# Kernel tuning notes

Hardware: AMD Instinct MI355X
Metric: run time of the kernel (lower is better)

## Reference

```python
import math
import jax, jax.numpy as jnp
import numpy as np

B, T, FDIM, ODIM = 16, 16, 64, 8
NQ, LAYERS, DEGREE = 10, 2, 3
NA = 4                      # ceil(log2(T))
TOT = NQ + NA               # 14 total wires
NROTS = 4 * NQ * LAYERS     # 80 params per timestep
QROTS = 4 * NQ              # 40 (qff circuit, 1 layer)
C64 = jnp.complex64


def ry_mat(t):
    c = jnp.cos(0.5 * t).astype(C64)
    s = jnp.sin(0.5 * t).astype(C64)
    return jnp.stack([jnp.stack([c, -s], -1), jnp.stack([s, c], -1)], -2)


def rz_mat(t):
    p = jnp.exp(-0.5j * t.astype(C64))
    q = jnp.exp(0.5j * t.astype(C64))
    z = jnp.zeros_like(p)
    return jnp.stack([jnp.stack([p, z], -1), jnp.stack([z, q], -1)], -2)


def crx_mat(t):
    c = jnp.cos(0.5 * t).astype(C64)
    s = (-1j) * jnp.sin(0.5 * t).astype(C64)
    z = jnp.zeros_like(c)
    o = jnp.ones_like(c)
    r0 = jnp.stack([o, z, z, z], -1)
    r1 = jnp.stack([z, o, z, z], -1)
    r2 = jnp.stack([z, z, c, s], -1)
    r3 = jnp.stack([z, z, s, c], -1)
    return jnp.stack([r0, r1, r2, r3], -2)


CNOT = jnp.array([[1, 0, 0, 0], [0, 1, 0, 0], [0, 0, 0, 1], [0, 0, 1, 0]], dtype=C64)


def apply_gate(state, U, wires):
    # state: (Be, 2,...,2) tensor; wire w lives on axis w+1. U: (2^k,2^k) or (Be,2^k,2^k)
    k = len(wires)
    axes = [w + 1 for w in wires]
    st = jnp.moveaxis(state, axes, list(range(1, k + 1)))
    shp = st.shape
    st = st.reshape(shp[0], 2 ** k, -1)
    eq = 'bij,bjr->bir' if U.ndim == 3 else 'ij,bjr->bir'
    st = jnp.einsum(eq, U, st).reshape(shp)
    return jnp.moveaxis(st, list(range(1, k + 1)), axes)


def sim14_seq(nq, layers):
    # gate sequence of Sim et al. circuit 14: RY ring, CRX ring, RY ring, CRX counter-ring
    seq, idx = [], 0
    for _ in range(layers):
        for i in range(nq):
            seq.append(('ry', (i,), idx)); idx += 1
        for i in range(nq - 1, -1, -1):
            seq.append(('crx', (i, (i + 1) % nq), idx)); idx += 1
        for i in range(nq):
            seq.append(('ry', (i,), idx)); idx += 1
        for i in [nq - 1] + list(range(nq - 1)):
            seq.append(('crx', (i, (i - 1) % nq), idx)); idx += 1
    return seq


def apply_sim14(state, params, layers, adjoint=False):
    seq = sim14_seq(NQ, layers)
    if adjoint:
        seq = seq[::-1]
    sign = -1.0 if adjoint else 1.0
    for kind, w, pidx in seq:
        th = sign * params[..., pidx]
        U = ry_mat(th) if kind == 'ry' else crx_mat(th)
        state = apply_gate(state, U, list(w))
    return state


def apply_prepare(state, prep_p, adjoint=False):
    # learnable PREPARE ansatz on ancilla wires NQ..NQ+NA-1 (n_prep_layers == NA)
    seq = []
    for ly in range(NA):
        for qi in range(NA):
            seq.append(('ry', NQ + qi, (ly, qi, 0)))
            seq.append(('rz', NQ + qi, (ly, qi, 1)))
        for i in range(NA - 1):
            seq.append(('cnot', (NQ + i, NQ + i + 1), None))
    if adjoint:
        seq = seq[::-1]
    sign = -1.0 if adjoint else 1.0
    for kind, w, pix in seq:
        if kind == 'cnot':
            state = apply_gate(state, CNOT, list(w))
        else:
            th = sign * prep_p[pix]
            U = ry_mat(th) if kind == 'ry' else rz_mat(th)
            state = apply_gate(state, U, [w])
    return state


def pcphase(state, phi):
    # PennyLane PCPhase(phi, dim=2^NQ, wires=anc+main): e^{+i phi} on ancilla==0 subspace, e^{-i phi} elsewhere
    st = state.reshape(B, 2 ** NQ, 2 ** NA)
    ph = jnp.exp(1j * phi.astype(C64))
    vec = jnp.where(jnp.arange(2 ** NA) == 0, ph, jnp.conj(ph))
    return (st * vec).reshape((B,) + (2,) * TOT)


def apply_select(state, ts_params, adjoint=False):
    # Select: apply sim14(ts_params[:, j]) on main wires when ancilla register == j
    # (T == 2^NA so there is no identity padding). Vectorized over batch x ancilla index.
    st = state.reshape(B, 2 ** NQ, 2 ** NA)
    st = jnp.moveaxis(st, 2, 1).reshape((B * T,) + (2,) * NQ)
    st = apply_sim14(st, ts_params.reshape(B * T, NROTS), LAYERS, adjoint)
    st = st.reshape(B, 2 ** NA, 2 ** NQ)
    return jnp.moveaxis(st, 1, 2).reshape((B,) + (2,) * TOT)


def expvals(state):
    # <X_i>, <Y_i>, <Z_i> on main wires, order X0..X9, Y0..Y9, Z0..Z9
    xs, ys, zs = [], [], []
    for i in range(NQ):
        s = jnp.moveaxis(state, i + 1, 1).reshape(B, 2, -1)
        s0, s1 = s[:, 0], s[:, 1]
        c = jnp.sum(jnp.conj(s0) * s1, axis=-1)
        xs.append(2.0 * jnp.real(c))
        ys.append(2.0 * jnp.imag(c))
        zs.append(jnp.sum(jnp.abs(s0) ** 2 - jnp.abs(s1) ** 2, axis=-1))
    return jnp.stack(xs + ys + zs, axis=1).astype(jnp.float32)  # (B, 3*NQ)


def make_pe():
    pos = np.arange(T, dtype=np.float32)[:, None]
    div = np.exp(np.arange(0, FDIM, 2, dtype=np.float32) * -(math.log(10000.0) / FDIM))
    pe = np.zeros((T, FDIM), np.float32)
    pe[:, 0::2] = np.sin(pos * div)
    pe[:, 1::2] = np.cos(pos * div[:FDIM // 2])
    return jnp.asarray(pe)


def setup_inputs():
    key = jax.random.key(0)
    ks = jax.random.split(key, 8)
    return {
        'x': jax.random.normal(ks[0], (B, FDIM, T), jnp.float32),
        'W_fp': jax.random.normal(ks[1], (NROTS, FDIM), jnp.float32) / math.sqrt(FDIM),
        'b_fp': jnp.zeros((NROTS,), jnp.float32),
        'prep_p': 0.1 * jax.random.normal(ks[2], (NA, NA, 2), jnp.float32),
        'sig_ang': 0.1 * jax.random.normal(ks[3], (DEGREE + 1,), jnp.float32),
        'qff_p': jax.random.uniform(ks[4], (QROTS,), jnp.float32),
        'W_out': jax.random.normal(ks[5], (ODIM, 3 * NQ), jnp.float32) / math.sqrt(3 * NQ),
        'b_out': jnp.zeros((ODIM,), jnp.float32),
    }


def reference(x, W_fp, b_fp, prep_p, sig_ang, qff_p, W_out, b_out):
    h = jnp.transpose(x, (0, 2, 1)) + make_pe()[None]          # (B, T, FDIM)
    ts = jax.nn.sigmoid(h @ W_fp.T + b_fp) * (2.0 * math.pi)    # (B, T, NROTS)
    # |0...0> on all 14 wires, batched
    psi = jnp.zeros((B, 2 ** TOT), C64).at[:, 0].set(1.0).reshape((B,) + (2,) * TOT)
    psi = pcphase(psi, sig_ang[0])
    for k in range(DEGREE):
        psi = apply_prepare(psi, prep_p, adjoint=False)
        psi = apply_select(psi, ts, adjoint=(k % 2 == 1))
        psi = apply_prepare(psi, prep_p, adjoint=True)
        psi = pcphase(psi, sig_ang[k + 1])
    psi = apply_sim14(psi, qff_p, layers=1, adjoint=False)      # QFF readout circuit
    exps = expvals(psi)                                         # (B, 30)
    return exps @ W_out.T + b_out                               # (B, ODIM)
```

## Files before the change

kernel.cpp:

```cpp
#include <hip/hip_runtime.h>
#include <math.h>
#include <utility>


typedef float v2f __attribute__((ext_vector_type(2)));

struct Gate { int ry; int tbit; int cbit; int pidx; };
struct GateTab { Gate g[40]; };

constexpr GateTab make_gates1() {
  GateTab tb{};
  int pos = 0, idx = 0;
  for (int i = 0; i < 10; ++i) { tb.g[pos] = Gate{1, 9 - i, -1, idx}; ++pos; ++idx; }
  for (int i = 9; i >= 0; --i) { tb.g[pos] = Gate{0, 9 - ((i + 1) % 10), 9 - i, idx}; ++pos; ++idx; }
  for (int i = 0; i < 10; ++i) { tb.g[pos] = Gate{1, 9 - i, -1, idx}; ++pos; ++idx; }
  for (int k = 0; k < 10; ++k) {
    int i = (k == 0) ? 9 : (k - 1);
    tb.g[pos] = Gate{0, 9 - ((i + 9) % 10), 9 - i, idx}; ++pos; ++idx;
  }
  return tb;
}
constexpr GateTab GTC = make_gates1();

__device__ __forceinline__ int insert_zero(int v, int p) {
  return ((v >> p) << (p + 1)) | (v & ((1 << p) - 1));
}
__device__ __forceinline__ float2 cmul(float2 A, float2 B) {
  return make_float2(A.x * B.x - A.y * B.y, A.x * B.y + A.y * B.x);
}
__device__ __forceinline__ float2 conj2(float2 A) { return make_float2(A.x, -A.y); }
__device__ __forceinline__ v2f vmk(float x, float y) { v2f r; r.x = x; r.y = y; return r; }

template<int XM>
__device__ __forceinline__ float lxor(float v) {
  if constexpr (XM == 1) {
    int r = __builtin_amdgcn_update_dpp(__float_as_int(v), __float_as_int(v),
                                        0xB1, 0xF, 0xF, true);
    return __int_as_float(r);
  } else if constexpr (XM == 2) {
    int r = __builtin_amdgcn_update_dpp(__float_as_int(v), __float_as_int(v),
                                        0x4E, 0xF, 0xF, true);
    return __int_as_float(r);
  } else if constexpr (XM == 8) {
    int r = __builtin_amdgcn_update_dpp(__float_as_int(v), __float_as_int(v),
                                        0x128, 0xF, 0xF, true);
    return __int_as_float(r);
  } else if constexpr (XM == 16) {
#if __has_builtin(__builtin_amdgcn_permlane16_swap)
    unsigned uv = __float_as_uint(v);
    auto r = __builtin_amdgcn_permlane16_swap(uv, uv, false, false);
    return __uint_as_float(r[0] ^ r[1] ^ uv);
#else
    return __shfl_xor(v, 16, 64);
#endif
  } else if constexpr (XM == 32) {
#if __has_builtin(__builtin_amdgcn_permlane32_swap)
    unsigned uv = __float_as_uint(v);
    auto r = __builtin_amdgcn_permlane32_swap(uv, uv, false, false);
    return __uint_as_float(r[0] ^ r[1] ^ uv);
#else
    return __shfl_xor(v, 32, 64);
#endif
  } else {
    return __shfl_xor(v, XM, 64);
  }
}
template<int XM>
__device__ __forceinline__ v2f lxor2(v2f v) {
  v2f r; r.x = lxor<XM>(v.x); r.y = lxor<XM>(v.y); return r;
}

__device__ __forceinline__ float wave_sum(float v) {
  v += lxor<1>(v);
  v += lxor<2>(v);
  v += lxor<4>(v);
  v += lxor<8>(v);
  v += lxor<16>(v);
  v += lxor<32>(v);
  return v;
}

struct alignas(128) GBar {
  unsigned cnt;
  unsigned gen;
  unsigned done;
  unsigned pad[29];
};
__device__ GBar g_gb[16];

__device__ __forceinline__ void group_barrier16(int b, int lane) {
  unsigned snap = __hip_atomic_load(&g_gb[b].gen, __ATOMIC_RELAXED, __HIP_MEMORY_SCOPE_AGENT);
  if (lane == 0) {
    unsigned old = __hip_atomic_fetch_add(&g_gb[b].cnt, 1u, __ATOMIC_ACQ_REL,
                                          __HIP_MEMORY_SCOPE_AGENT);
    if ((old & 15u) == 15u)
      __hip_atomic_store(&g_gb[b].gen, snap + 1u, __ATOMIC_RELEASE,
                         __HIP_MEMORY_SCOPE_AGENT);
  }
  while (__hip_atomic_load(&g_gb[b].gen, __ATOMIC_RELAXED, __HIP_MEMORY_SCOPE_AGENT) == snap)
    __builtin_amdgcn_s_sleep(1);
  (void)__hip_atomic_load(&g_gb[b].gen, __ATOMIC_ACQUIRE, __HIP_MEMORY_SCOPE_AGENT);
}

template<int P>
__device__ __forceinline__ void ry_gate(v2f (&a)[16], float c, float s, int lane) {
  if constexpr (P < 4) {
    constexpr int m = 1 << P;
#pragma unroll
    for (int r0 = 0; r0 < 16; ++r0) {
      if (!(r0 & m)) {
        int r1 = r0 | m;
        v2f a0 = a[r0], a1 = a[r1];
        a[r0] = c * a0 - s * a1;
        a[r1] = s * a0 + c * a1;
      }
    }
  } else {
    constexpr int xm = 1 << (P - 4);
    bool up = (lane >> (P - 4)) & 1;
    float sg = up ? s : -s;
#pragma unroll
    for (int r = 0; r < 16; ++r) {
      v2f wv = lxor2<xm>(a[r]);
      a[r] = c * a[r] + sg * wv;
    }
  }
}

template<int P, int Q>
__device__ __forceinline__ void crx_gate(v2f (&a)[16], float c, float s, int lane) {
  if constexpr (P < 4) {
    constexpr int m = 1 << P;
#pragma unroll
    for (int r0 = 0; r0 < 16; ++r0) {
      if (!(r0 & m)) {
        int r1 = r0 | m;
        bool act;
        if constexpr (Q < 4) act = (r0 >> Q) & 1;
        else act = (lane >> (Q - 4)) & 1;
        if (act) {
          v2f a0 = a[r0], a1 = a[r1];
          a[r0] = c * a0 + s * vmk(a1.y, -a1.x);
          a[r1] = c * a1 + s * vmk(a0.y, -a0.x);
        }
      }
    }
  } else {
    constexpr int xm = 1 << (P - 4);
#pragma unroll
    for (int r = 0; r < 16; ++r) {
      v2f wv = lxor2<xm>(a[r]);
      bool act;
      if constexpr (Q < 4) act = (r >> Q) & 1;
      else act = (lane >> (Q - 4)) & 1;
      if (act) a[r] = c * a[r] + s * vmk(wv.y, -wv.x);
    }
  }
}

template<bool ADJ, int G>
__device__ __forceinline__ void one_gate(v2f (&a)[16], const float2 (&sc)[40], int lane) {
  constexpr Gate g = GTC.g[ADJ ? (39 - G) : G];
  float2 scv = sc[g.pidx];
  float s = ADJ ? -scv.x : scv.x;
  float c = scv.y;
  if constexpr (g.ry != 0) ry_gate<g.tbit>(a, c, s, lane);
  else crx_gate<g.tbit, g.cbit>(a, c, s, lane);
}

template<bool ADJ, int... I>
__device__ __forceinline__ void run_layer_impl(v2f (&a)[16], const float2 (&sc)[40],
                                               int lane, std::integer_sequence<int, I...>) {
  (one_gate<ADJ, I>(a, sc, lane), ...);
}

template<bool ADJ>
__device__ __forceinline__ void run_layer(v2f (&a)[16], const float2* sc, int lane) {
  float2 rsc[40];
#pragma unroll
  for (int i = 0; i < 40; ++i) rsc[i] = sc[i];
  run_layer_impl<ADJ>(a, rsc, lane, std::make_integer_sequence<int, 40>{});
}

__global__ __launch_bounds__(256, 1) void k_fused(const float* __restrict__ x,
                                                  const float* __restrict__ W_fp,
                                                  const float* __restrict__ b_fp,
                                                  const float* __restrict__ prep,
                                                  const float* __restrict__ sig,
                                                  const float* __restrict__ qff,
                                                  const float* __restrict__ W_out,
                                                  const float* __restrict__ b_out,
                                                  float* __restrict__ out,
                                                  float4* __restrict__ part1,
                                                  float4* __restrict__ part2,
                                                  float* __restrict__ sv) {
  int blk = blockIdx.x;
  int b = blk >> 2, sub = blk & 3;
  int tid = threadIdx.x;
  int w = tid >> 6, lane = tid & 63;
  int aa = sub * 4 + w;

  __shared__ __align__(16) float h[4][64];
  __shared__ float2 scs[4][80];
  __shared__ float2 qscs[40];
  __shared__ float2 ps[32];
  __shared__ float2 es[4];
  __shared__ float2 u0s[16];
  __shared__ float4 R[2][512];

  if (sub == 0 && w == 0 && lane < 30) sv[b * 30 + lane] = 0.f;

  {
    int f = lane, k = f >> 1;
    float div = expf(-(float)(2 * k) * (logf(10000.f) / 64.f));
    float ang = (float)aa * div;
    float pe = (f & 1) ? cosf(ang) : sinf(ang);
    h[w][f] = x[(b * 64 + f) * 16 + aa] + pe;
  }
  if (w == 0) {
    if (lane < 32) {
      float s, c;
      sincosf(0.5f * prep[lane], &s, &c);
      ps[lane] = make_float2(s, c);
    } else if (lane < 36) {
      float s, c;
      sincosf(sig[lane - 32], &s, &c);
      es[lane - 32] = make_float2(c, s);
    }
  } else if (w == 1 && lane < 40) {
    float s, c;
    sincosf(0.5f * qff[lane], &s, &c);
    qscs[lane] = make_float2(s, c);
  }
  __syncthreads();

  if (w == 0) {
    float2 v[16];
#pragma unroll
    for (int i = 0; i < 16; ++i) v[i] = make_float2(i == 0 ? 1.f : 0.f, 0.f);
#pragma unroll 1
    for (int ly = 0; ly < 4; ++ly) {
#pragma unroll
      for (int qi = 0; qi < 4; ++qi) {
        int p = 3 - qi;
        float2 rc = ps[ly * 8 + qi * 2 + 0];
        {
          float s = rc.x, c = rc.y;
#pragma unroll
          for (int m = 0; m < 8; ++m) {
            int a0 = insert_zero(m, p), a1 = a0 | (1 << p);
            float2 t0 = v[a0], t1 = v[a1];
            v[a0] = make_float2(c * t0.x - s * t1.x, c * t0.y - s * t1.y);
            v[a1] = make_float2(s * t0.x + c * t1.x, s * t0.y + c * t1.y);
          }
        }
        rc = ps[ly * 8 + qi * 2 + 1];
        {
          float s = rc.x, c = rc.y;
#pragma unroll
          for (int m = 0; m < 8; ++m) {
            int a0 = insert_zero(m, p), a1 = a0 | (1 << p);
            float2 t0 = v[a0], t1 = v[a1];
            v[a0] = make_float2(c * t0.x + s * t0.y, c * t0.y - s * t0.x);
            v[a1] = make_float2(c * t1.x - s * t1.y, c * t1.y + s * t1.x);
          }
        }
      }
#pragma unroll
      for (int i = 0; i < 3; ++i) {
        int pc = 3 - i, pt = 2 - i;
#pragma unroll
        for (int m = 0; m < 4; ++m) {
          int mm = insert_zero(m, pt);
          mm = insert_zero(mm, pc);
          int a0 = mm | (1 << pc), a1 = a0 | (1 << pt);
          float2 t0 = v[a0], t1 = v[a1];
          v[a0] = t1; v[a1] = t0;
        }
      }
    }
    if (lane == 0) {
#pragma unroll
      for (int i = 0; i < 16; ++i) u0s[i] = v[i];
    }
  }

  {
    const float4* h4 = (const float4*)&h[w][0];
    for (int j = lane; j < 80; j += 64) {
      float acc = b_fp[j];
      const float4* w4 = (const float4*)(W_fp + j * 64);
#pragma unroll
      for (int k4 = 0; k4 < 16; ++k4) {
        float4 hh = h4[k4], ww = w4[k4];
        acc += hh.x * ww.x + hh.y * ww.y + hh.z * ww.z + hh.w * ww.w;
      }
      float sg = 1.f / (1.f + expf(-acc));
      float s, c;
      sincosf(sg * 3.14159265358979323846f, &s, &c);
      scs[w][j] = make_float2(s, c);
    }
  }
  __syncthreads();

  float2 u0aa = u0s[aa];
  float2 e0 = es[0], e1 = es[1], e2 = es[2];
  float2 m0  = cmul(u0aa, e0);
  float2 cu0 = conj2(u0aa);
  float2 ceA = conj2(e1);
  float2 wA  = make_float2(-2.f * e1.y * u0aa.y, 2.f * e1.y * u0aa.x);
  float2 ceB = conj2(e2);
  float2 wB  = make_float2(-2.f * e2.y * u0aa.y, 2.f * e2.y * u0aa.x);

  const float2* sc = &scs[w][0];
  v2f a[16];
#pragma unroll
  for (int r = 0; r < 16; ++r) a[r] = vmk(0.f, 0.f);
  if (lane == 0) a[0] = vmk(m0.x, m0.y);

#pragma unroll 1
  for (int ph = 0; ph < 7; ++ph) {
    if (ph == 2 || ph == 4) {
      float2 ce = (ph == 2) ? ceA : ceB;
      float2 wk = (ph == 2) ? wA : wB;
      float4* part = (ph == 2) ? part1 : part2;

      __syncthreads();
      if (w < 2) {
#pragma unroll
        for (int q = 0; q < 8; ++q) {
          float2 p0 = cmul(cu0, make_float2(a[2 * q].x, a[2 * q].y));
          float2 p1 = cmul(cu0, make_float2(a[2 * q + 1].x, a[2 * q + 1].y));
          R[w][q * 64 + lane] = make_float4(p0.x, p0.y, p1.x, p1.y);
        }
      }
      __syncthreads();
      if (w >= 2) {
#pragma unroll
        for (int q = 0; q < 8; ++q) {
          float4 v = R[w - 2][q * 64 + lane];
          float2 p0 = cmul(cu0, make_float2(a[2 * q].x, a[2 * q].y));
          float2 p1 = cmul(cu0, make_float2(a[2 * q + 1].x, a[2 * q + 1].y));
          R[w - 2][q * 64 + lane] =
              make_float4(v.x + p0.x, v.y + p0.y, v.z + p1.x, v.w + p1.y);
        }
      }
      __syncthreads();
#pragma unroll
      for (int qq = 0; qq < 2; ++qq) {
        int q = w * 2 + qq;
        float4 v0 = R[0][q * 64 + lane];
        float4 v1 = R[1][q * 64 + lane];
        part[(size_t)(b * 4 + sub) * 512 + q * 64 + lane] =
            make_float4(v0.x + v1.x, v0.y + v1.y, v0.z + v1.z, v0.w + v1.w);
      }
      group_barrier16(b, lane);

      float4 s4[8];
#pragma unroll
      for (int q = 0; q < 8; ++q) {
        float4 v0 = R[0][q * 64 + lane];
        float4 v1 = R[1][q * 64 + lane];
        s4[q] = make_float4(v0.x + v1.x, v0.y + v1.y, v0.z + v1.z, v0.w + v1.w);
      }
#pragma unroll 1
      for (int o = 1; o < 4; ++o) {
        int so = (sub + o) & 3;
        const float4* pp = part + (size_t)(b * 4 + so) * 512 + lane;
#pragma unroll
        for (int q = 0; q < 8; ++q) {
          float4 v = pp[q * 64];
          s4[q].x += v.x; s4[q].y += v.y; s4[q].z += v.z; s4[q].w += v.w;
        }
      }
#pragma unroll
      for (int q = 0; q < 8; ++q) {
        v2f a0 = a[2 * q], a1 = a[2 * q + 1];
        a[2 * q] = vmk(ce.x * a0.x - ce.y * a0.y + wk.x * s4[q].x - wk.y * s4[q].y,
                       ce.x * a0.y + ce.y * a0.x + wk.x * s4[q].y + wk.y * s4[q].x);
        a[2 * q + 1] = vmk(ce.x * a1.x - ce.y * a1.y + wk.x * s4[q].z - wk.y * s4[q].w,
                           ce.x * a1.y + ce.y * a1.x + wk.x * s4[q].w + wk.y * s4[q].z);
      }
    }
    const float2* scp;
    if (ph == 6) scp = &qscs[0];
    else scp = sc + ((ph == 1 || ph == 2 || ph == 5) ? 40 : 0);
    if (ph == 2 || ph == 3) run_layer<true>(a, scp, lane);
    else                    run_layer<false>(a, scp, lane);
  }

  {
    float obs[30];
#pragma unroll
    for (int p = 0; p <= 9; ++p) {
      int i = 9 - p;
      float cr = 0.f, ci = 0.f, zz = 0.f;
      if (p < 4) {
        int m = 1 << p;
#pragma unroll
        for (int r0 = 0; r0 < 16; ++r0) {
          if (!(r0 & m)) {
            v2f A0 = a[r0], A1 = a[r0 | m];
            cr += A0.x * A1.x + A0.y * A1.y;
            ci += A0.x * A1.y - A0.y * A1.x;
            zz += (A0.x * A0.x + A0.y * A0.y) - (A1.x * A1.x + A1.y * A1.y);
          }
        }
      } else {
        int xm = 1 << (p - 4);
        bool up = (lane >> (p - 4)) & 1;
#pragma unroll
        for (int r = 0; r < 16; ++r) {
          float wx = __shfl_xor(a[r].x, xm, 64);
          float wy = __shfl_xor(a[r].y, xm, 64);
          float n2 = a[r].x * a[r].x + a[r].y * a[r].y;
          if (!up) {
            cr += a[r].x * wx + a[r].y * wy;
            ci += a[r].x * wy - a[r].y * wx;
            zz += n2;
          } else {
            zz -= n2;
          }
        }
      }
      obs[i] = 2.f * cr;
      obs[10 + i] = 2.f * ci;
      obs[20 + i] = zz;
    }
#pragma unroll
    for (int j = 0; j < 30; ++j) obs[j] = wave_sum(obs[j]);

    float* Rf = (float*)R;
    __syncthreads();
    if (lane == 0) {
#pragma unroll
      for (int j = 0; j < 30; ++j) Rf[w * 30 + j] = obs[j];
    }
    __syncthreads();
    if (w == 0) {
      if (lane < 30) {
        float v = Rf[0 * 30 + lane] + Rf[1 * 30 + lane] +
                  Rf[2 * 30 + lane] + Rf[3 * 30 + lane];
        atomicAdd(&sv[b * 30 + lane], v);
      }
      int lastflag = 0;
      if (lane == 0) {
        unsigned old = __hip_atomic_fetch_add(&g_gb[b].done, 1u, __ATOMIC_ACQ_REL,
                                              __HIP_MEMORY_SCOPE_AGENT);
        lastflag = ((old & 3u) == 3u) ? 1 : 0;
      }
      lastflag = __shfl(lastflag, 0, 64);
      if (lastflag) {
        (void)__hip_atomic_load(&g_gb[b].done, __ATOMIC_ACQUIRE, __HIP_MEMORY_SCOPE_AGENT);
        if (lane < 8) {
          float acc = b_out[lane];
#pragma unroll
          for (int j = 0; j < 30; ++j) acc += W_out[lane * 30 + j] * sv[b * 30 + j];
          out[b * 8 + lane] = acc;
        }
      }
    }
  }
}

extern "C" void kernel_launch(void* const* d_in, const int* in_sizes, int n_in,
                              void* d_out, int out_size, void* d_ws, size_t ws_size,
                              hipStream_t stream) {
  const float* x     = (const float*)d_in[0];
  const float* W_fp  = (const float*)d_in[1];
  const float* b_fp  = (const float*)d_in[2];
  const float* prep  = (const float*)d_in[3];
  const float* sig   = (const float*)d_in[4];
  const float* qff   = (const float*)d_in[5];
  const float* W_out = (const float*)d_in[6];
  const float* b_out = (const float*)d_in[7];
  float* out = (float*)d_out;
  (void)in_sizes; (void)n_in; (void)out_size;

  char* ws = (char*)d_ws;
  const size_t SZ_PART = (size_t)64 * 512 * 16;
  float4* part1 = (float4*)ws;
  float4* part2 = (float4*)(ws + SZ_PART);
  float*  sv    = (float*)(ws + 2 * SZ_PART);
  (void)ws_size;

  k_fused<<<dim3(64), dim3(256), 0, stream>>>(x, W_fp, b_fp, prep, sig, qff,
                                              W_out, b_out, out, part1, part2, sv);
}
```

Baseline: 163.5 us.

## Split each 1024-amplitude state across two waves, doubling grid to 128 blocks

Each ancilla-branch state vector, previously held by one wave as 16 amplitudes per lane, is now split across a pair of waves with 8 amplitudes per lane. One qubit is mapped to the wave index, and gates on that qubit exchange amplitudes through double-buffered LDS with a block barrier. The grid doubles to 128 blocks, with a 32-way cross-block barrier per batch and 8-way partial-sum reduction. The per-wave compute and register pressure halve, at the cost of extra __syncthreads per wave-bit gate, a larger group barrier, and more global partial traffic. A ds_swizzle path is added for the xor-4 lane exchange.

```diff
diff --git a/kernel.cpp b/kernel.cpp
--- a/kernel.cpp
+++ b/kernel.cpp
@@ -22,6 +22,10 @@
 }
 constexpr GateTab GTC = make_gates1();
 
+constexpr int lanebit_of(int P) {
+  return P == 3 ? 0 : P == 4 ? 1 : P == 5 ? 2 : P == 7 ? 3 : P == 8 ? 4 : 5;
+}
+
 __device__ __forceinline__ int insert_zero(int v, int p) {
   return ((v >> p) << (p + 1)) | (v & ((1 << p) - 1));
 }
@@ -40,6 +44,9 @@
   } else if constexpr (XM == 2) {
     int r = __builtin_amdgcn_update_dpp(__float_as_int(v), __float_as_int(v),
                                         0x4E, 0xF, 0xF, true);
+    return __int_as_float(r);
+  } else if constexpr (XM == 4) {
+    int r = __builtin_amdgcn_ds_swizzle(__float_as_int(v), 0x101F);
     return __int_as_float(r);
   } else if constexpr (XM == 8) {
     int r = __builtin_amdgcn_update_dpp(__float_as_int(v), __float_as_int(v),
@@ -53,7 +60,7 @@
 #else
     return __shfl_xor(v, 16, 64);
 #endif
-  } else if constexpr (XM == 32) {
+  } else {
 #if __has_builtin(__builtin_amdgcn_permlane32_swap)
     unsigned uv = __float_as_uint(v);
     auto r = __builtin_amdgcn_permlane32_swap(uv, uv, false, false);
@@ -61,8 +68,6 @@
 #else
     return __shfl_xor(v, 32, 64);
 #endif
-  } else {
-    return __shfl_xor(v, XM, 64);
   }
 }
 template<int XM>
@@ -88,12 +93,12 @@
 };
 __device__ GBar g_gb[16];
 
-__device__ __forceinline__ void group_barrier16(int b, int lane) {
+__device__ __forceinline__ void group_barrier32(int b, int lane) {
   unsigned snap = __hip_atomic_load(&g_gb[b].gen, __ATOMIC_RELAXED, __HIP_MEMORY_SCOPE_AGENT);
   if (lane == 0) {
     unsigned old = __hip_atomic_fetch_add(&g_gb[b].cnt, 1u, __ATOMIC_ACQ_REL,
                                           __HIP_MEMORY_SCOPE_AGENT);
-    if ((old & 15u) == 15u)
+    if ((old & 31u) == 31u)
       __hip_atomic_store(&g_gb[b].gen, snap + 1u, __ATOMIC_RELEASE,
                          __HIP_MEMORY_SCOPE_AGENT);
   }
@@ -102,12 +107,35 @@
   (void)__hip_atomic_load(&g_gb[b].gen, __ATOMIC_ACQUIRE, __HIP_MEMORY_SCOPE_AGENT);
 }
 
+struct Ctx {
+  int lane, wbit;
+  int buf;
+  float2* xo0; float2* xo1;
+  const float2* xp0; const float2* xp1;
+};
+
+__device__ __forceinline__ const float2* xchg(v2f (&a)[8], Ctx& ctx) {
+  float2* wo = ctx.buf ? ctx.xo1 : ctx.xo0;
+#pragma unroll
+  for (int r = 0; r < 8; ++r) wo[r] = make_float2(a[r].x, a[r].y);
+  __syncthreads();
+  const float2* wp = ctx.buf ? ctx.xp1 : ctx.xp0;
+  ctx.buf ^= 1;
+  return wp;
+}
+
+template<int Q>
+__device__ __forceinline__ bool act_of(int r, int lane) {
+  if constexpr (Q < 3) return (r >> Q) & 1;
+  else { constexpr int lb = lanebit_of(Q); return (lane >> lb) & 1; }
+}
+
 template<int P>
-__device__ __forceinline__ void ry_gate(v2f (&a)[16], float c, float s, int lane) {
-  if constexpr (P < 4) {
+__device__ __forceinline__ void ry_gate(v2f (&a)[8], float c, float s, Ctx& ctx) {
+  if constexpr (P < 3) {
     constexpr int m = 1 << P;
 #pragma unroll
-    for (int r0 = 0; r0 < 16; ++r0) {
+    for (int r0 = 0; r0 < 8; ++r0) {
       if (!(r0 & m)) {
         int r1 = r0 | m;
         v2f a0 = a[r0], a1 = a[r1];
@@ -115,30 +143,69 @@
         a[r1] = s * a0 + c * a1;
       }
     }
+  } else if constexpr (P == 6) {
+    const float2* wp = xchg(a, ctx);
+    float sg = ctx.wbit ? s : -s;
+#pragma unroll
+    for (int r = 0; r < 8; ++r) {
+      float2 w = wp[r];
+      a[r] = c * a[r] + sg * vmk(w.x, w.y);
+    }
   } else {
-    constexpr int xm = 1 << (P - 4);
-    bool up = (lane >> (P - 4)) & 1;
+    constexpr int xm = 1 << lanebit_of(P);
+    bool up = (ctx.lane >> lanebit_of(P)) & 1;
     float sg = up ? s : -s;
 #pragma unroll
-    for (int r = 0; r < 16; ++r) {
+    for (int r = 0; r < 8; ++r) {
       v2f wv = lxor2<xm>(a[r]);
       a[r] = c * a[r] + sg * wv;
     }
   }
 }
 
-template<int P, int Q>
-__device__ __forceinline__ void crx_gate(v2f (&a)[16], float c, float s, int lane) {
-  if constexpr (P < 4) {
+template<int P>
+__device__ __forceinline__ void crx_all(v2f (&a)[8], float c, float s, Ctx& ctx) {
+  if constexpr (P < 3) {
     constexpr int m = 1 << P;
 #pragma unroll
-    for (int r0 = 0; r0 < 16; ++r0) {
+    for (int r0 = 0; r0 < 8; ++r0) {
       if (!(r0 & m)) {
         int r1 = r0 | m;
-        bool act;
-        if constexpr (Q < 4) act = (r0 >> Q) & 1;
-        else act = (lane >> (Q - 4)) & 1;
-        if (act) {
+        v2f a0 = a[r0], a1 = a[r1];
+        a[r0] = c * a0 + s * vmk(a1.y, -a1.x);
+        a[r1] = c * a1 + s * vmk(a0.y, -a0.x);
+      }
+    }
+  } else {
+    constexpr int xm = 1 << lanebit_of(P);
+#pragma unroll
+    for (int r = 0; r < 8; ++r) {
+      v2f wv = lxor2<xm>(a[r]);
+      a[r] = c * a[r] + s * vmk(wv.y, -wv.x);
+    }
+  }
+}
+
+template<int P, int Q>
+__device__ __forceinline__ void crx_gate(v2f (&a)[8], float c, float s, Ctx& ctx) {
+  if constexpr (Q == 6) {
+    if (ctx.wbit) crx_all<P>(a, c, s, ctx);
+  } else if constexpr (P == 6) {
+    const float2* wp = xchg(a, ctx);
+#pragma unroll
+    for (int r = 0; r < 8; ++r) {
+      if (act_of<Q>(r, ctx.lane)) {
+        float2 w = wp[r];
+        a[r] = c * a[r] + s * vmk(w.y, -w.x);
+      }
+    }
+  } else if constexpr (P < 3) {
+    constexpr int m = 1 << P;
+#pragma unroll
+    for (int r0 = 0; r0 < 8; ++r0) {
+      if (!(r0 & m)) {
+        int r1 = r0 | m;
+        if (act_of<Q>(r0, ctx.lane)) {
           v2f a0 = a[r0], a1 = a[r1];
           a[r0] = c * a0 + s * vmk(a1.y, -a1.x);
           a[r1] = c * a1 + s * vmk(a0.y, -a0.x);
@@ -146,40 +213,37 @@
       }
     }
   } else {
-    constexpr int xm = 1 << (P - 4);
-#pragma unroll
-    for (int r = 0; r < 16; ++r) {
+    constexpr int xm = 1 << lanebit_of(P);
+#pragma unroll
+    for (int r = 0; r < 8; ++r) {
       v2f wv = lxor2<xm>(a[r]);
-      bool act;
-      if constexpr (Q < 4) act = (r >> Q) & 1;
-      else act = (lane >> (Q - 4)) & 1;
-      if (act) a[r] = c * a[r] + s * vmk(wv.y, -wv.x);
+      if (act_of<Q>(r, ctx.lane)) a[r] = c * a[r] + s * vmk(wv.y, -wv.x);
     }
   }
 }
 
 template<bool ADJ, int G>
-__device__ __forceinline__ void one_gate(v2f (&a)[16], const float2 (&sc)[40], int lane) {
+__device__ __forceinline__ void one_gate(v2f (&a)[8], const float2 (&sc)[40], Ctx& ctx) {
   constexpr Gate g = GTC.g[ADJ ? (39 - G) : G];
   float2 scv = sc[g.pidx];
   float s = ADJ ? -scv.x : scv.x;
   float c = scv.y;
-  if constexpr (g.ry != 0) ry_gate<g.tbit>(a, c, s, lane);
-  else crx_gate<g.tbit, g.cbit>(a, c, s, lane);
+  if constexpr (g.ry != 0) ry_gate<g.tbit>(a, c, s, ctx);
+  else crx_gate<g.tbit, g.cbit>(a, c, s, ctx);
 }
 
 template<bool ADJ, int... I>
-__device__ __forceinline__ void run_layer_impl(v2f (&a)[16], const float2 (&sc)[40],
-                                               int lane, std::integer_sequence<int, I...>) {
-  (one_gate<ADJ, I>(a, sc, lane), ...);
+__device__ __forceinline__ void run_layer_impl(v2f (&a)[8], const float2 (&sc)[40],
+                                               Ctx& ctx, std::integer_sequence<int, I...>) {
+  (one_gate<ADJ, I>(a, sc, ctx), ...);
 }
 
 template<bool ADJ>
-__device__ __forceinline__ void run_layer(v2f (&a)[16], const float2* sc, int lane) {
+__device__ __forceinline__ void run_layer(v2f (&a)[8], const float2* sc, Ctx& ctx) {
   float2 rsc[40];
 #pragma unroll
   for (int i = 0; i < 40; ++i) rsc[i] = sc[i];
-  run_layer_impl<ADJ>(a, rsc, lane, std::make_integer_sequence<int, 40>{});
+  run_layer_impl<ADJ>(a, rsc, ctx, std::make_integer_sequence<int, 40>{});
 }
 
 __global__ __launch_bounds__(256, 1) void k_fused(const float* __restrict__ x,
@@ -195,42 +259,44 @@
                                                   float4* __restrict__ part2,
                                                   float* __restrict__ sv) {
   int blk = blockIdx.x;
-  int b = blk >> 2, sub = blk & 3;
+  int b = blk >> 3, sub = blk & 7;
   int tid = threadIdx.x;
   int w = tid >> 6, lane = tid & 63;
-  int aa = sub * 4 + w;
-
-  __shared__ __align__(16) float h[4][64];
-  __shared__ float2 scs[4][80];
+  int c = w >> 1, wbit = w & 1;
+  int aa = sub * 2 + c;
+
+  __shared__ float2 X[2][2][2][64][8];
+  __shared__ float2 R[1024];
+  __shared__ __align__(16) float h[2][64];
+  __shared__ float2 scs[2][80];
   __shared__ float2 qscs[40];
   __shared__ float2 ps[32];
   __shared__ float2 es[4];
   __shared__ float2 u0s[16];
-  __shared__ float4 R[2][512];
 
   if (sub == 0 && w == 0 && lane < 30) sv[b * 30 + lane] = 0.f;
 
-  {
+  if (wbit == 0) {
     int f = lane, k = f >> 1;
     float div = expf(-(float)(2 * k) * (logf(10000.f) / 64.f));
     float ang = (float)aa * div;
     float pe = (f & 1) ? cosf(ang) : sinf(ang);
-    h[w][f] = x[(b * 64 + f) * 16 + aa] + pe;
-  }
-  if (w == 0) {
+    h[c][f] = x[(b * 64 + f) * 16 + aa] + pe;
+  }
+  if (w == 1) {
     if (lane < 32) {
-      float s, c;
-      sincosf(0.5f * prep[lane], &s, &c);
-      ps[lane] = make_float2(s, c);
+      float s, cc;
+      sincosf(0.5f * prep[lane], &s, &cc);
+      ps[lane] = make_float2(s, cc);
     } else if (lane < 36) {
-      float s, c;
-      sincosf(sig[lane - 32], &s, &c);
-      es[lane - 32] = make_float2(c, s);
-    }
-  } else if (w == 1 && lane < 40) {
-    float s, c;
-    sincosf(0.5f * qff[lane], &s, &c);
-    qscs[lane] = make_float2(s, c);
+      float s, cc;
+      sincosf(sig[lane - 32], &s, &cc);
+      es[lane - 32] = make_float2(cc, s);
+    }
+  } else if (w == 3 && lane < 40) {
+    float s, cc;
+    sincosf(0.5f * qff[lane], &s, &cc);
+    qscs[lane] = make_float2(s, cc);
   }
   __syncthreads();
 
@@ -245,24 +311,24 @@
         int p = 3 - qi;
         float2 rc = ps[ly * 8 + qi * 2 + 0];
         {
-          float s = rc.x, c = rc.y;
+          float s = rc.x, cc = rc.y;
 #pragma unroll
           for (int m = 0; m < 8; ++m) {
             int a0 = insert_zero(m, p), a1 = a0 | (1 << p);
             float2 t0 = v[a0], t1 = v[a1];
-            v[a0] = make_float2(c * t0.x - s * t1.x, c * t0.y - s * t1.y);
-            v[a1] = make_float2(s * t0.x + c * t1.x, s * t0.y + c * t1.y);
+            v[a0] = make_float2(cc * t0.x - s * t1.x, cc * t0.y - s * t1.y);
+            v[a1] = make_float2(s * t0.x + cc * t1.x, s * t0.y + cc * t1.y);
           }
         }
         rc = ps[ly * 8 + qi * 2 + 1];
         {
-          float s = rc.x, c = rc.y;
+          float s = rc.x, cc = rc.y;
 #pragma unroll
           for (int m = 0; m < 8; ++m) {
             int a0 = insert_zero(m, p), a1 = a0 | (1 << p);
             float2 t0 = v[a0], t1 = v[a1];
-            v[a0] = make_float2(c * t0.x + s * t0.y, c * t0.y - s * t0.x);
-            v[a1] = make_float2(c * t1.x - s * t1.y, c * t1.y + s * t1.x);
+            v[a0] = make_float2(cc * t0.x + s * t0.y, cc * t0.y - s * t0.x);
+            v[a1] = make_float2(cc * t1.x - s * t1.y, cc * t1.y + s * t1.x);
           }
         }
       }
@@ -285,21 +351,20 @@
     }
   }
 
-  {
-    const float4* h4 = (const float4*)&h[w][0];
-    for (int j = lane; j < 80; j += 64) {
-      float acc = b_fp[j];
-      const float4* w4 = (const float4*)(W_fp + j * 64);
-#pragma unroll
-      for (int k4 = 0; k4 < 16; ++k4) {
-        float4 hh = h4[k4], ww = w4[k4];
-        acc += hh.x * ww.x + hh.y * ww.y + hh.z * ww.z + hh.w * ww.w;
-      }
-      float sg = 1.f / (1.f + expf(-acc));
-      float s, c;
-      sincosf(sg * 3.14159265358979323846f, &s, &c);
-      scs[w][j] = make_float2(s, c);
-    }
+  if (lane < 40) {
+    int j = wbit * 40 + lane;
+    const float4* h4 = (const float4*)&h[c][0];
+    float acc = b_fp[j];
+    const float4* w4 = (const float4*)(W_fp + j * 64);
+#pragma unroll
+    for (int k4 = 0; k4 < 16; ++k4) {
+      float4 hh = h4[k4], ww = w4[k4];
+      acc += hh.x * ww.x + hh.y * ww.y + hh.z * ww.z + hh.w * ww.w;
+    }
+    float sg = 1.f / (1.f + expf(-acc));
+    float s, cc;
+    sincosf(sg * 3.14159265358979323846f, &s, &cc);
+    scs[c][j] = make_float2(s, cc);
   }
   __syncthreads();
 
@@ -312,11 +377,18 @@
   float2 ceB = conj2(e2);
   float2 wB  = make_float2(-2.f * e2.y * u0aa.y, 2.f * e2.y * u0aa.x);
 
-  const float2* sc = &scs[w][0];
-  v2f a[16];
-#pragma unroll
-  for (int r = 0; r < 16; ++r) a[r] = vmk(0.f, 0.f);
-  if (lane == 0) a[0] = vmk(m0.x, m0.y);
+  Ctx ctx;
+  ctx.lane = lane; ctx.wbit = wbit; ctx.buf = 0;
+  ctx.xo0 = &X[c][0][wbit][lane][0];
+  ctx.xo1 = &X[c][1][wbit][lane][0];
+  ctx.xp0 = &X[c][0][wbit ^ 1][lane][0];
+  ctx.xp1 = &X[c][1][wbit ^ 1][lane][0];
+
+  const float2* sc = &scs[c][0];
+  v2f a[8];
+#pragma unroll
+  for (int r = 0; r < 8; ++r) a[r] = vmk(0.f, 0.f);
+  if (wbit == 0 && lane == 0) a[0] = vmk(m0.x, m0.y);
 
 #pragma unroll 1
   for (int ph = 0; ph < 7; ++ph) {
@@ -324,69 +396,62 @@
       float2 ce = (ph == 2) ? ceA : ceB;
       float2 wk = (ph == 2) ? wA : wB;
       float4* part = (ph == 2) ? part1 : part2;
+      int base = wbit * 512 + lane * 8;
 
       __syncthreads();
-      if (w < 2) {
-#pragma unroll
-        for (int q = 0; q < 8; ++q) {
-          float2 p0 = cmul(cu0, make_float2(a[2 * q].x, a[2 * q].y));
-          float2 p1 = cmul(cu0, make_float2(a[2 * q + 1].x, a[2 * q + 1].y));
-          R[w][q * 64 + lane] = make_float4(p0.x, p0.y, p1.x, p1.y);
-        }
+      if (c == 0) {
+#pragma unroll
+        for (int r = 0; r < 8; ++r)
+          R[base + r] = cmul(cu0, make_float2(a[r].x, a[r].y));
       }
       __syncthreads();
-      if (w >= 2) {
-#pragma unroll
-        for (int q = 0; q < 8; ++q) {
-          float4 v = R[w - 2][q * 64 + lane];
-          float2 p0 = cmul(cu0, make_float2(a[2 * q].x, a[2 * q].y));
-          float2 p1 = cmul(cu0, make_float2(a[2 * q + 1].x, a[2 * q + 1].y));
-          R[w - 2][q * 64 + lane] =
-              make_float4(v.x + p0.x, v.y + p0.y, v.z + p1.x, v.w + p1.y);
+      if (c == 1) {
+#pragma unroll
+        for (int r = 0; r < 8; ++r) {
+          float2 v = R[base + r];
+          float2 p = cmul(cu0, make_float2(a[r].x, a[r].y));
+          R[base + r] = make_float2(v.x + p.x, v.y + p.y);
         }
       }
       __syncthreads();
-#pragma unroll
-      for (int qq = 0; qq < 2; ++qq) {
-        int q = w * 2 + qq;
-        float4 v0 = R[0][q * 64 + lane];
-        float4 v1 = R[1][q * 64 + lane];
-        part[(size_t)(b * 4 + sub) * 512 + q * 64 + lane] =
-            make_float4(v0.x + v1.x, v0.y + v1.y, v0.z + v1.z, v0.w + v1.w);
-      }
-      group_barrier16(b, lane);
-
-      float4 s4[8];
-#pragma unroll
-      for (int q = 0; q < 8; ++q) {
-        float4 v0 = R[0][q * 64 + lane];
-        float4 v1 = R[1][q * 64 + lane];
-        s4[q] = make_float4(v0.x + v1.x, v0.y + v1.y, v0.z + v1.z, v0.w + v1.w);
+      {
+        float4* dst = part + (size_t)(b * 8 + sub) * 512;
+        const float4* src = (const float4*)R;
+        dst[tid] = src[tid];
+        dst[tid + 256] = src[tid + 256];
+      }
+      group_barrier32(b, lane);
+
+      float4 sA[4];
+#pragma unroll
+      for (int q = 0; q < 4; ++q) {
+        float2 lo = R[base + 2 * q], hi = R[base + 2 * q + 1];
+        sA[q] = make_float4(lo.x, lo.y, hi.x, hi.y);
       }
 #pragma unroll 1
-      for (int o = 1; o < 4; ++o) {
-        int so = (sub + o) & 3;
-        const float4* pp = part + (size_t)(b * 4 + so) * 512 + lane;
-#pragma unroll
-        for (int q = 0; q < 8; ++q) {
-          float4 v = pp[q * 64];
-          s4[q].x += v.x; s4[q].y += v.y; s4[q].z += v.z; s4[q].w += v.w;
-        }
-      }
-#pragma unroll
-      for (int q = 0; q < 8; ++q) {
+      for (int o = 1; o < 8; ++o) {
+        int so = (sub + o) & 7;
+        const float4* pp = part + (size_t)(b * 8 + so) * 512 + wbit * 256 + lane * 4;
+#pragma unroll
+        for (int q = 0; q < 4; ++q) {
+          float4 v = pp[q];
+          sA[q].x += v.x; sA[q].y += v.y; sA[q].z += v.z; sA[q].w += v.w;
+        }
+      }
+#pragma unroll
+      for (int q = 0; q < 4; ++q) {
         v2f a0 = a[2 * q], a1 = a[2 * q + 1];
-        a[2 * q] = vmk(ce.x * a0.x - ce.y * a0.y + wk.x * s4[q].x - wk.y * s4[q].y,
-                       ce.x * a0.y + ce.y * a0.x + wk.x * s4[q].y + wk.y * s4[q].x);
-        a[2 * q + 1] = vmk(ce.x * a1.x - ce.y * a1.y + wk.x * s4[q].z - wk.y * s4[q].w,
-                           ce.x * a1.y + ce.y * a1.x + wk.x * s4[q].w + wk.y * s4[q].z);
+        a[2 * q] = vmk(ce.x * a0.x - ce.y * a0.y + wk.x * sA[q].x - wk.y * sA[q].y,
+                       ce.x * a0.y + ce.y * a0.x + wk.x * sA[q].y + wk.y * sA[q].x);
+        a[2 * q + 1] = vmk(ce.x * a1.x - ce.y * a1.y + wk.x * sA[q].z - wk.y * sA[q].w,
+                           ce.x * a1.y + ce.y * a1.x + wk.x * sA[q].w + wk.y * sA[q].z);
       }
     }
     const float2* scp;
     if (ph == 6) scp = &qscs[0];
     else scp = sc + ((ph == 1 || ph == 2 || ph == 5) ? 40 : 0);
-    if (ph == 2 || ph == 3) run_layer<true>(a, scp, lane);
-    else                    run_layer<false>(a, scp, lane);
+    if (ph == 2 || ph == 3) run_layer<true>(a, scp, ctx);
+    else                    run_layer<false>(a, scp, ctx);
   }
 
   {
@@ -395,10 +460,10 @@
     for (int p = 0; p <= 9; ++p) {
       int i = 9 - p;
       float cr = 0.f, ci = 0.f, zz = 0.f;
-      if (p < 4) {
+      if (p < 3) {
         int m = 1 << p;
 #pragma unroll
-        for (int r0 = 0; r0 < 16; ++r0) {
+        for (int r0 = 0; r0 < 8; ++r0) {
           if (!(r0 & m)) {
             v2f A0 = a[r0], A1 = a[r0 | m];
             cr += A0.x * A1.x + A0.y * A1.y;
@@ -406,11 +471,31 @@
             zz += (A0.x * A0.x + A0.y * A0.y) - (A1.x * A1.x + A1.y * A1.y);
           }
         }
+      } else if (p == 6) {
+        float2* wo = ctx.buf ? ctx.xo1 : ctx.xo0;
+#pragma unroll
+        for (int r = 0; r < 8; ++r) wo[r] = make_float2(a[r].x, a[r].y);
+        __syncthreads();
+        const float2* wp = ctx.buf ? ctx.xp1 : ctx.xp0;
+        ctx.buf ^= 1;
+#pragma unroll
+        for (int r = 0; r < 8; ++r) {
+          float n2 = a[r].x * a[r].x + a[r].y * a[r].y;
+          if (wbit == 0) {
+            float2 ww = wp[r];
+            cr += a[r].x * ww.x + a[r].y * ww.y;
+            ci += a[r].x * ww.y - a[r].y * ww.x;
+            zz += n2;
+          } else {
+            zz -= n2;
+          }
+        }
       } else {
-        int xm = 1 << (p - 4);
-        bool up = (lane >> (p - 4)) & 1;
-#pragma unroll
-        for (int r = 0; r < 16; ++r) {
+        int lb = (p == 3) ? 0 : (p == 4) ? 1 : (p == 5) ? 2 : (p == 7) ? 3 : (p == 8) ? 4 : 5;
+        int xm = 1 << lb;
+        bool up = (lane >> lb) & 1;
+#pragma unroll
+        for (int r = 0; r < 8; ++r) {
           float wx = __shfl_xor(a[r].x, xm, 64);
           float wy = __shfl_xor(a[r].y, xm, 64);
           float n2 = a[r].x * a[r].x + a[r].y * a[r].y;
@@ -447,7 +532,7 @@
       if (lane == 0) {
         unsigned old = __hip_atomic_fetch_add(&g_gb[b].done, 1u, __ATOMIC_ACQ_REL,
                                               __HIP_MEMORY_SCOPE_AGENT);
-        lastflag = ((old & 3u) == 3u) ? 1 : 0;
+        lastflag = ((old & 7u) == 7u) ? 1 : 0;
       }
       lastflag = __shfl(lastflag, 0, 64);
       if (lastflag) {
@@ -478,12 +563,12 @@
   (void)in_sizes; (void)n_in; (void)out_size;
 
   char* ws = (char*)d_ws;
-  const size_t SZ_PART = (size_t)64 * 512 * 16;
+  const size_t SZ_PART = (size_t)128 * 512 * 16;
   float4* part1 = (float4*)ws;
   float4* part2 = (float4*)(ws + SZ_PART);
   float*  sv    = (float*)(ws + 2 * SZ_PART);
   (void)ws_size;
 
-  k_fused<<<dim3(64), dim3(256), 0, stream>>>(x, W_fp, b_fp, prep, sig, qff,
-                                              W_out, b_out, out, part1, part2, sv);
-}
+  k_fused<<<dim3(128), dim3(256), 0, stream>>>(x, W_fp, b_fp, prep, sig, qff,
+                                               W_out, b_out, out, part1, part2, sv);
+}
```

After: 161.7 us. No clear change (-1.1%).
